# Kernel tuning notes

Measured on AMD Instinct MI355X. Metric: run time of the kernel, lower is better.

## Reference

```python
import jax, jax.numpy as jnp
import numpy as np

B, S, H, D = 8, 4096, 32, 128
DM = H * D

def setup_inputs() -> dict:
    key = jax.random.key(0)
    k1, k2, k3, k4, k5 = jax.random.split(key, 5)
    return {
        "hidden_state": jax.random.normal(k1, (B, DM), dtype=jnp.float32),
        "key_states": jax.random.normal(k2, (B, S, DM), dtype=jnp.float32),
        "value_states": jax.random.normal(k3, (B, S, DM), dtype=jnp.float32),
        "Wq": jax.random.normal(k4, (DM, DM), dtype=jnp.float32) * 0.02,
        "bq": jax.random.normal(k5, (DM,), dtype=jnp.float32) * 0.02,
    }

def reference(hidden_state, key_states, value_states, Wq, bq):
    # q projection: torch Linear -> x @ W^T + b
    q = (hidden_state @ Wq.T + bq).reshape(B, H, D)          # [B,H,D]
    k = key_states.reshape(B, S, H, D)                        # [B,S,H,D]
    v = value_states.reshape(B, S, H, D)
    # NOTE: original module applies no 1/sqrt(D) scaling
    scores = jnp.einsum('bhd,bshd->bhs', q, k)                # [B,H,S]
    probs = jax.nn.softmax(scores, axis=-1)
    out = jnp.einsum('bhs,bshd->bhd', probs, v)               # [B,H,D]
    return out[:, :, None, :]                                 # [B,H,1,D] to match torch output
```

## Files before the change

kernel.cpp:

```cpp
#include <hip/hip_runtime.h>

#define B 8
#define S 4096
#define H 32
#define D 128
#define DM 4096

#define NT 1024
#define WAVES 16

__global__ __launch_bounds__(256) void qproj_kernel(
    const float* __restrict__ hidden, const float* __restrict__ Wq,
    const float* __restrict__ bq, float* __restrict__ qout)
{
    const int lane = threadIdx.x & 63;
    const int wave = threadIdx.x >> 6;
    const int j0 = (blockIdx.x * 4 + wave) * 2;
    const int j1 = j0 + 1;

    const float4* __restrict__ w0 = (const float4*)(Wq + (size_t)j0 * DM);
    const float4* __restrict__ w1 = (const float4*)(Wq + (size_t)j1 * DM);
    const float4* __restrict__ hid = (const float4*)hidden;

    float a0[B], a1[B];
#pragma unroll
    for (int b = 0; b < B; ++b) { a0[b] = 0.f; a1[b] = 0.f; }

#pragma unroll
    for (int i = 0; i < DM / (4 * 64); ++i) {
        const int idx = lane + 64 * i;
        const float4 wv0 = w0[idx];
        const float4 wv1 = w1[idx];
#pragma unroll
        for (int b = 0; b < B; ++b) {
            const float4 hv = hid[b * (DM / 4) + idx];
            a0[b] += wv0.x * hv.x + wv0.y * hv.y + wv0.z * hv.z + wv0.w * hv.w;
            a1[b] += wv1.x * hv.x + wv1.y * hv.y + wv1.z * hv.z + wv1.w * hv.w;
        }
    }
#pragma unroll
    for (int b = 0; b < B; ++b) {
#pragma unroll
        for (int mk = 1; mk <= 32; mk <<= 1) {
            a0[b] += __shfl_xor(a0[b], mk);
            a1[b] += __shfl_xor(a1[b], mk);
        }
    }
    if (lane == 0) {
        const float bias0 = bq[j0];
        const float bias1 = bq[j1];
#pragma unroll
        for (int b = 0; b < B; ++b) {
            qout[b * DM + j0] = a0[b] + bias0;
            qout[b * DM + j1] = a1[b] + bias1;
        }
    }
}

__global__ __launch_bounds__(NT) void attn_kernel(
    const float* __restrict__ kptr, const float* __restrict__ vptr,
    const float* __restrict__ qws, float* __restrict__ out)
{
    __shared__ float sc[S];
    __shared__ float red[WAVES];
    __shared__ float outp[WAVES][D];

    const int tid  = threadIdx.x;
    const int lane = tid & 63;
    const int wave = tid >> 6;
    const int g    = lane >> 5;
    const int l    = lane & 31;
    const int b    = blockIdx.x >> 5;
    const int h    = blockIdx.x & (H - 1);

    const size_t base = ((size_t)b * S * H + h) * D;
    const float* kb = kptr + base;
    const float* vb = vptr + base;

    const float4 q4 = *(const float4*)(qws + (size_t)b * DM + h * D + 4 * l);

#pragma unroll 2
    for (int it = 0; it < S / 32; ++it) {
        const int s = it * 32 + 2 * wave + g;
        const float4 k4 = *(const float4*)(kb + (size_t)s * DM + 4 * l);
        float p = q4.x * k4.x + q4.y * k4.y + q4.z * k4.z + q4.w * k4.w;
        p += __shfl_xor(p, 16);
        p += __shfl_xor(p, 8);
        p += __shfl_xor(p, 4);
        p += __shfl_xor(p, 2);
        p += __shfl_xor(p, 1);
        if (l == 0) sc[s] = p;
    }
    __syncthreads();

    float m = -3.4e38f;
    for (int i = tid; i < S; i += NT) m = fmaxf(m, sc[i]);
#pragma unroll
    for (int mk = 1; mk <= 32; mk <<= 1) m = fmaxf(m, __shfl_xor(m, mk));
    if (lane == 0) red[wave] = m;
    __syncthreads();
    float M = red[0];
#pragma unroll
    for (int w = 1; w < WAVES; ++w) M = fmaxf(M, red[w]);

    float lsum = 0.f;
    for (int i = tid; i < S; i += NT) {
        const float e = __expf(sc[i] - M);
        sc[i] = e;
        lsum += e;
    }
#pragma unroll
    for (int mk = 1; mk <= 32; mk <<= 1) lsum += __shfl_xor(lsum, mk);
    __syncthreads();
    if (lane == 0) red[wave] = lsum;
    __syncthreads();
    float tot = 0.f;
#pragma unroll
    for (int w = 0; w < WAVES; ++w) tot += red[w];
    const float inv = 1.0f / tot;

    float4 acc = make_float4(0.f, 0.f, 0.f, 0.f);
    const int s0 = wave * (S / WAVES);
#pragma unroll 2
    for (int i = 0; i < S / WAVES; i += 2) {
        const int s = s0 + i + g;
        const float p = sc[s];
        const float4 v4 = *(const float4*)(vb + (size_t)s * DM + 4 * l);
        acc.x += p * v4.x;
        acc.y += p * v4.y;
        acc.z += p * v4.z;
        acc.w += p * v4.w;
    }
    acc.x += __shfl_xor(acc.x, 32);
    acc.y += __shfl_xor(acc.y, 32);
    acc.z += __shfl_xor(acc.z, 32);
    acc.w += __shfl_xor(acc.w, 32);
    if (g == 0) *(float4*)(&outp[wave][4 * l]) = acc;
    __syncthreads();

    if (tid < D) {
        float r = 0.f;
#pragma unroll
        for (int w = 0; w < WAVES; ++w) r += outp[w][tid];
        out[(size_t)(b * H + h) * D + tid] = r * inv;
    }
}

extern "C" void kernel_launch(void* const* d_in, const int* in_sizes, int n_in,
                              void* d_out, int out_size, void* d_ws, size_t ws_size,
                              hipStream_t stream)
{
    const float* hidden = (const float*)d_in[0];
    const float* keys   = (const float*)d_in[1];
    const float* vals   = (const float*)d_in[2];
    const float* Wq     = (const float*)d_in[3];
    const float* bq     = (const float*)d_in[4];
    float* outp = (float*)d_out;
    float* qws  = (float*)d_ws;

    qproj_kernel<<<DM / 8, 256, 0, stream>>>(hidden, Wq, bq, qws);
    attn_kernel<<<B * H, NT, 0, stream>>>(keys, vals, qws, outp);
}
```

Before: 216.5 us.

## Split attention over sequence chunks with a combine kernel, widen qproj grid

Splits each (batch, head) attention across 4 sequence chunks so the grid grows from 256 to 1024 blocks of 512 threads. Each block writes a partial output, max and sum, and a new combine kernel merges them with log-sum-exp rescaling. The q projection now uses one output row per wave, doubling its block count. The goal is better CU occupancy on the bandwidth-bound K/V streaming, at the cost of an extra kernel launch and a small partial buffer round-trip.

```diff
diff --git a/kernel.cpp b/kernel.cpp
--- a/kernel.cpp
+++ b/kernel.cpp
@@ -6,8 +6,11 @@
 #define D 128
 #define DM 4096
 
-#define NT 1024
-#define WAVES 16
+#define SPLIT 4
+#define SC (S / SPLIT)
+#define NT 512
+#define NWAVE 8
+#define PSTR 132
 
 __global__ __launch_bounds__(256) void qproj_kernel(
     const float* __restrict__ hidden, const float* __restrict__ Wq,
@@ -15,73 +18,64 @@
 {
     const int lane = threadIdx.x & 63;
     const int wave = threadIdx.x >> 6;
-    const int j0 = (blockIdx.x * 4 + wave) * 2;
-    const int j1 = j0 + 1;
+    const int j = blockIdx.x * 4 + wave;
 
-    const float4* __restrict__ w0 = (const float4*)(Wq + (size_t)j0 * DM);
-    const float4* __restrict__ w1 = (const float4*)(Wq + (size_t)j1 * DM);
+    const float4* __restrict__ w   = (const float4*)(Wq + (size_t)j * DM);
     const float4* __restrict__ hid = (const float4*)hidden;
 
-    float a0[B], a1[B];
+    float a[B];
 #pragma unroll
-    for (int b = 0; b < B; ++b) { a0[b] = 0.f; a1[b] = 0.f; }
+    for (int b = 0; b < B; ++b) a[b] = 0.f;
 
-#pragma unroll
+#pragma unroll 4
     for (int i = 0; i < DM / (4 * 64); ++i) {
         const int idx = lane + 64 * i;
-        const float4 wv0 = w0[idx];
-        const float4 wv1 = w1[idx];
+        const float4 wv = w[idx];
 #pragma unroll
         for (int b = 0; b < B; ++b) {
             const float4 hv = hid[b * (DM / 4) + idx];
-            a0[b] += wv0.x * hv.x + wv0.y * hv.y + wv0.z * hv.z + wv0.w * hv.w;
-            a1[b] += wv1.x * hv.x + wv1.y * hv.y + wv1.z * hv.z + wv1.w * hv.w;
+            a[b] += wv.x * hv.x + wv.y * hv.y + wv.z * hv.z + wv.w * hv.w;
         }
     }
 #pragma unroll
     for (int b = 0; b < B; ++b) {
 #pragma unroll
-        for (int mk = 1; mk <= 32; mk <<= 1) {
-            a0[b] += __shfl_xor(a0[b], mk);
-            a1[b] += __shfl_xor(a1[b], mk);
-        }
+        for (int mk = 1; mk <= 32; mk <<= 1) a[b] += __shfl_xor(a[b], mk);
     }
     if (lane == 0) {
-        const float bias0 = bq[j0];
-        const float bias1 = bq[j1];
+        const float bias = bq[j];
 #pragma unroll
-        for (int b = 0; b < B; ++b) {
-            qout[b * DM + j0] = a0[b] + bias0;
-            qout[b * DM + j1] = a1[b] + bias1;
-        }
+        for (int b = 0; b < B; ++b) qout[b * DM + j] = a[b] + bias;
     }
 }
 
-__global__ __launch_bounds__(NT) void attn_kernel(
+__global__ __launch_bounds__(NT) void attn_partial(
     const float* __restrict__ kptr, const float* __restrict__ vptr,
-    const float* __restrict__ qws, float* __restrict__ out)
+    const float* __restrict__ qws, float* __restrict__ part)
 {
-    __shared__ float sc[S];
-    __shared__ float red[WAVES];
-    __shared__ float outp[WAVES][D];
+    __shared__ float sc[SC];
+    __shared__ float red[NWAVE];
+    __shared__ float outp[NWAVE][D];
 
     const int tid  = threadIdx.x;
     const int lane = tid & 63;
     const int wave = tid >> 6;
+    const int gid  = tid >> 5;
     const int g    = lane >> 5;
     const int l    = lane & 31;
-    const int b    = blockIdx.x >> 5;
-    const int h    = blockIdx.x & (H - 1);
+    const int c    = blockIdx.x & (SPLIT - 1);
+    const int h    = (blockIdx.x >> 2) & (H - 1);
+    const int b    = blockIdx.x >> 7;
 
-    const size_t base = ((size_t)b * S * H + h) * D;
+    const size_t base = (((size_t)b * S + (size_t)c * SC) * H + h) * D;
     const float* kb = kptr + base;
     const float* vb = vptr + base;
 
     const float4 q4 = *(const float4*)(qws + (size_t)b * DM + h * D + 4 * l);
 
-#pragma unroll 2
-    for (int it = 0; it < S / 32; ++it) {
-        const int s = it * 32 + 2 * wave + g;
+#pragma unroll 4
+    for (int it = 0; it < SC / 16; ++it) {
+        const int s = it * 16 + gid;
         const float4 k4 = *(const float4*)(kb + (size_t)s * DM + 4 * l);
         float p = q4.x * k4.x + q4.y * k4.y + q4.z * k4.z + q4.w * k4.w;
         p += __shfl_xor(p, 16);
@@ -94,17 +88,19 @@
     __syncthreads();
 
     float m = -3.4e38f;
-    for (int i = tid; i < S; i += NT) m = fmaxf(m, sc[i]);
+#pragma unroll
+    for (int i = tid; i < SC; i += NT) m = fmaxf(m, sc[i]);
 #pragma unroll
     for (int mk = 1; mk <= 32; mk <<= 1) m = fmaxf(m, __shfl_xor(m, mk));
     if (lane == 0) red[wave] = m;
     __syncthreads();
     float M = red[0];
 #pragma unroll
-    for (int w = 1; w < WAVES; ++w) M = fmaxf(M, red[w]);
+    for (int w = 1; w < NWAVE; ++w) M = fmaxf(M, red[w]);
 
     float lsum = 0.f;
-    for (int i = tid; i < S; i += NT) {
+#pragma unroll
+    for (int i = tid; i < SC; i += NT) {
         const float e = __expf(sc[i] - M);
         sc[i] = e;
         lsum += e;
@@ -116,13 +112,12 @@
     __syncthreads();
     float tot = 0.f;
 #pragma unroll
-    for (int w = 0; w < WAVES; ++w) tot += red[w];
-    const float inv = 1.0f / tot;
+    for (int w = 0; w < NWAVE; ++w) tot += red[w];
 
     float4 acc = make_float4(0.f, 0.f, 0.f, 0.f);
-    const int s0 = wave * (S / WAVES);
-#pragma unroll 2
-    for (int i = 0; i < S / WAVES; i += 2) {
+    const int s0 = wave * (SC / NWAVE);
+#pragma unroll 4
+    for (int i = 0; i < SC / NWAVE; i += 2) {
         const int s = s0 + i + g;
         const float p = sc[s];
         const float4 v4 = *(const float4*)(vb + (size_t)s * DM + 4 * l);
@@ -138,12 +133,36 @@
     if (g == 0) *(float4*)(&outp[wave][4 * l]) = acc;
     __syncthreads();
 
+    float* rec = part + ((size_t)(b * H + h) * SPLIT + c) * PSTR;
     if (tid < D) {
         float r = 0.f;
 #pragma unroll
-        for (int w = 0; w < WAVES; ++w) r += outp[w][tid];
-        out[(size_t)(b * H + h) * D + tid] = r * inv;
+        for (int w = 0; w < NWAVE; ++w) r += outp[w][tid];
+        rec[tid] = r;
+    } else if (tid == D) {
+        rec[D] = M;
+        rec[D + 1] = tot;
     }
+}
+
+__global__ __launch_bounds__(128) void combine_kernel(
+    const float* __restrict__ part, float* __restrict__ out)
+{
+    const int bh = blockIdx.x;
+    const int d  = threadIdx.x;
+    const float* rec = part + (size_t)bh * SPLIT * PSTR;
+
+    float M = -3.4e38f;
+#pragma unroll
+    for (int c = 0; c < SPLIT; ++c) M = fmaxf(M, rec[c * PSTR + D]);
+    float denom = 0.f, o = 0.f;
+#pragma unroll
+    for (int c = 0; c < SPLIT; ++c) {
+        const float w = __expf(rec[c * PSTR + D] - M);
+        denom += w * rec[c * PSTR + D + 1];
+        o     += w * rec[c * PSTR + d];
+    }
+    out[(size_t)bh * D + d] = o / denom;
 }
 
 extern "C" void kernel_launch(void* const* d_in, const int* in_sizes, int n_in,
@@ -157,7 +176,9 @@
     const float* bq     = (const float*)d_in[4];
     float* outp = (float*)d_out;
     float* qws  = (float*)d_ws;
+    float* part = qws + (size_t)B * DM;
 
-    qproj_kernel<<<DM / 8, 256, 0, stream>>>(hidden, Wq, bq, qws);
-    attn_kernel<<<B * H, NT, 0, stream>>>(keys, vals, qws, outp);
+    qproj_kernel<<<DM / 4, 256, 0, stream>>>(hidden, Wq, bq, qws);
+    attn_partial<<<B * H * SPLIT, NT, 0, stream>>>(keys, vals, qws, part);
+    combine_kernel<<<B * H, 128, 0, stream>>>(part, outp);
 }
```

New measurement: 219.5 us. No clear change (+1.4%).
